# Performance work log

Measured on AMD Instinct MI355X. Metric: run time of the kernel, lower is better.

Reference implementation:

```python
import jax, jax.numpy as jnp
import numpy as np

N = 100000
E = 3200000
F_IN = 512
HID = 16
NUM_CLASSES = 2
NUM_GRAPHS = 256


def setup_inputs() -> dict:
    key = jax.random.key(0)
    k = jax.random.split(key, 8)
    x = jax.random.normal(k[0], (N, F_IN), dtype=jnp.float32)
    edge_index = jax.random.randint(k[1], (2, E), 0, N, dtype=jnp.int64)
    batch = jnp.sort(jax.random.randint(k[2], (N,), 0, NUM_GRAPHS, dtype=jnp.int64))
    # Glorot init like PyG GCNConv, biases zero-init
    W1 = jax.random.normal(k[3], (F_IN, HID), dtype=jnp.float32) * (2.0 / (F_IN + HID)) ** 0.5
    b1 = jnp.zeros((HID,), dtype=jnp.float32)
    W2 = jax.random.normal(k[4], (HID, NUM_CLASSES), dtype=jnp.float32) * (2.0 / (HID + NUM_CLASSES)) ** 0.5
    b2 = jnp.zeros((NUM_CLASSES,), dtype=jnp.float32)
    return {"x": x, "W1": W1, "b1": b1, "W2": W2, "b2": b2,
            "edge_index": edge_index, "batch": batch}


def _gcn_conv(x, W, b, src, dst, n):
    # PyG GCNConv: linear first, add self loops, symmetric deg^-1/2 normalization,
    # scatter-add messages from src to dst, then bias.
    h = x @ W                                        # [N, out]
    loops = jnp.arange(n, dtype=src.dtype)
    s = jnp.concatenate([src, loops])                # [E+N]
    d = jnp.concatenate([dst, loops])                # [E+N]
    deg = jax.ops.segment_sum(jnp.ones_like(d, dtype=h.dtype), d, num_segments=n)
    dinv = jax.lax.rsqrt(deg)                        # deg >= 1 due to self loops
    norm = dinv[s] * dinv[d]                         # [E+N]
    out = jax.ops.segment_sum(norm[:, None] * h[s], d, num_segments=n)
    return out + b


def reference(x, W1, b1, W2, b2, edge_index, batch):
    src, dst = edge_index[0], edge_index[1]
    h = jax.nn.relu(_gcn_conv(x, W1, b1, src, dst, N))
    h = _gcn_conv(h, W2, b2, src, dst, N)
    # global_mean_pool over graph ids
    sums = jax.ops.segment_sum(h, batch, num_segments=NUM_GRAPHS)
    counts = jax.ops.segment_sum(jnp.ones((N,), dtype=h.dtype), batch, num_segments=NUM_GRAPHS)
    pooled = sums / jnp.maximum(counts, 1.0)[:, None]  # [G, num_classes]
    return jax.nn.log_softmax(pooled, axis=1)
```

## Files before the change

### kernel.cpp

```cpp
#include <hip/hip_runtime.h>
#include <hip/hip_fp16.h>

#define N_NODES 100000
#define N_EDGES 3200000
#define F_INN 512
#define NGR 256
#define BSH 6
#define NBIN 1563
#define KBB 256
#define CHUNK (N_EDGES / KBB)
#define CAP 2560

typedef __attribute__((ext_vector_type(8))) short bf16x8;
typedef __attribute__((ext_vector_type(4))) float f32x4;

__device__ __forceinline__ uint f2bf2(float a, float b) {
  uint ua = __float_as_uint(a), ub = __float_as_uint(b);
  uint ra = (ua + 0x7FFF + ((ua >> 16) & 1)) >> 16;
  uint rb = (ub + 0x7FFF + ((ub >> 16) & 1)) >> 16;
  return ra | (rb << 16);
}

__global__ __launch_bounds__(512) void k_bin(const int* __restrict__ ei,
                                             int* __restrict__ bincur,
                                             int* __restrict__ rec,
                                             const float* __restrict__ W,
                                             ushort* __restrict__ Wt) {
  if (blockIdx.x == KBB) {
    for (int tid = threadIdx.x; tid < 16 * 512; tid += 512) {
      int n = tid >> 9;
      int k = tid & 511;
      uint u = __float_as_uint(W[k * 16 + n]);
      Wt[tid] = (ushort)((u + 0x7FFF + ((u >> 16) & 1)) >> 16);
    }
    return;
  }
  __shared__ int h[NBIN];
  __shared__ int base[NBIN];
  for (int t = threadIdx.x; t < NBIN; t += 512) h[t] = 0;
  __syncthreads();
  int e0 = blockIdx.x * CHUNK;
  for (int i = threadIdx.x; i < CHUNK; i += 512)
    atomicAdd(&h[ei[N_EDGES + e0 + i] >> BSH], 1);
  __syncthreads();
  for (int t = threadIdx.x; t < NBIN; t += 512) {
    int c = h[t];
    base[t] = t * CAP + (c ? atomicAdd(&bincur[t], c) : 0);
    h[t] = 0;
  }
  __syncthreads();
  for (int i = threadIdx.x; i < CHUNK; i += 512) {
    int s = ei[e0 + i];
    int d = ei[N_EDGES + e0 + i];
    int k = d >> BSH;
    int pos = base[k] + atomicAdd(&h[k], 1);
    rec[pos] = (s << BSH) | (d & 63);
  }
}

__global__ __launch_bounds__(256) void k_binsort(const int* __restrict__ rec,
                                                 const int* __restrict__ bincur,
                                                 int* __restrict__ rec2,
                                                 int* __restrict__ nstart,
                                                 int* __restrict__ ncnt,
                                                 float* __restrict__ dinv) {
  __shared__ int h[64], excl[64], cur[64];
  int k = blockIdx.x, t = threadIdx.x;
  if (t < 64) h[t] = 0;
  __syncthreads();
  int start = k * CAP;
  int end = start + bincur[k];
  for (int r = start + t; r < end; r += 256)
    atomicAdd(&h[rec[r] & 63], 1);
  __syncthreads();
  if (t < 64) {
    int v = h[t];
    int sc = v;
#pragma unroll
    for (int o = 1; o < 64; o <<= 1) {
      int u = __shfl_up(sc, o);
      if (t >= o) sc += u;
    }
    int ex = sc - v;
    excl[t] = ex;
    cur[t] = 0;
    int node = (k << BSH) + t;
    if (node < N_NODES) {
      nstart[node] = start + ex;
      ncnt[node] = v;
      dinv[node] = rsqrtf((float)v + 1.0f);
    }
  }
  __syncthreads();
  for (int r = start + t; r < end; r += 256) {
    int v = rec[r];
    int dl = v & 63;
    int pos = start + excl[dl] + atomicAdd(&cur[dl], 1);
    rec2[pos] = v;
  }
}

__global__ __launch_bounds__(256) void k_gemm1(const float* __restrict__ X,
                                               const ushort* __restrict__ Wt,
                                               const float* __restrict__ dinv,
                                               __half* __restrict__ T1h) {
  const int t = threadIdx.x;
  const int lane = t & 63;
  const int w = t >> 6;
  const int c16 = lane & 15;
  const int g = lane >> 4;
  const int arow = blockIdx.x * 64 + w * 16 + c16;
  const bool rv = arow < N_NODES;
  const float* xrow = X + (size_t)arow * F_INN + g * 8;
  const ushort* brow = Wt + c16 * 512 + g * 8;

  f32x4 acc = {0.f, 0.f, 0.f, 0.f};
#pragma unroll
  for (int ks = 0; ks < 16; ++ks) {
    float4 v0 = rv ? *(const float4*)(xrow + ks * 32)     : make_float4(0.f, 0.f, 0.f, 0.f);
    float4 v1 = rv ? *(const float4*)(xrow + ks * 32 + 4) : make_float4(0.f, 0.f, 0.f, 0.f);
    uint au[4] = { f2bf2(v0.x, v0.y), f2bf2(v0.z, v0.w),
                   f2bf2(v1.x, v1.y), f2bf2(v1.z, v1.w) };
    bf16x8 a = *(const bf16x8*)au;
    bf16x8 b = *(const bf16x8*)(brow + ks * 32);
    acc = __builtin_amdgcn_mfma_f32_16x16x32_bf16(a, b, acc, 0, 0, 0);
  }

  int rbase = blockIdx.x * 64 + w * 16 + g * 4;
#pragma unroll
  for (int j = 0; j < 4; ++j) {
    int r = rbase + j;
    if (r < N_NODES)
      T1h[(size_t)r * 16 + c16] = __float2half(dinv[r] * acc[j]);
  }
}

__global__ __launch_bounds__(256) void k_agg1(const int* __restrict__ rec2,
                                              const int* __restrict__ bincur,
                                              const int* __restrict__ nstart,
                                              const int* __restrict__ ncnt,
                                              const float* __restrict__ dinv,
                                              const __half* __restrict__ T1h,
                                              const float* __restrict__ b1,
                                              const float* __restrict__ W2,
                                              float* __restrict__ T2) {
  __shared__ float accs[64 * 17];
  __shared__ int recs[CAP];
  int k = blockIdx.x, t = threadIdx.x;
  int n0 = k << BSH;
  int cnt = bincur[k];
  for (int i = t; i < cnt; i += 256) recs[i] = rec2[k * CAP + i];
  int node = n0 + (t >> 2);
  int q = t & 3;
  bool nvalid = node < N_NODES;
  float a0 = 0.f, a1 = 0.f, a2 = 0.f, a3 = 0.f;
  int r = 0, e = 0;
  if (nvalid) {
    r = nstart[node] - k * CAP;
    e = r + ncnt[node];
    uint2 u = *(const uint2*)(T1h + (size_t)node * 16 + q * 4);
    float2 f0 = __half22float2(*reinterpret_cast<__half2*>(&u.x));
    float2 f1 = __half22float2(*reinterpret_cast<__half2*>(&u.y));
    a0 = f0.x; a1 = f0.y; a2 = f1.x; a3 = f1.y;
  }
  __syncthreads();
  for (; r + 1 < e; r += 2) {
    int v0 = recs[r], v1 = recs[r + 1];
    uint2 ua = *(const uint2*)(T1h + (size_t)(v0 >> BSH) * 16 + q * 4);
    uint2 ub = *(const uint2*)(T1h + (size_t)(v1 >> BSH) * 16 + q * 4);
    float2 fa0 = __half22float2(*reinterpret_cast<__half2*>(&ua.x));
    float2 fa1 = __half22float2(*reinterpret_cast<__half2*>(&ua.y));
    float2 fb0 = __half22float2(*reinterpret_cast<__half2*>(&ub.x));
    float2 fb1 = __half22float2(*reinterpret_cast<__half2*>(&ub.y));
    a0 += fa0.x + fb0.x; a1 += fa0.y + fb0.y;
    a2 += fa1.x + fb1.x; a3 += fa1.y + fb1.y;
  }
  if (r < e) {
    int v = recs[r];
    uint2 u = *(const uint2*)(T1h + (size_t)(v >> BSH) * 16 + q * 4);
    float2 f0 = __half22float2(*reinterpret_cast<__half2*>(&u.x));
    float2 f1 = __half22float2(*reinterpret_cast<__half2*>(&u.y));
    a0 += f0.x; a1 += f0.y; a2 += f1.x; a3 += f1.y;
  }
  float dd = nvalid ? dinv[node] : 0.f;
  float* rowp = &accs[(t >> 2) * 17 + q * 4];
  rowp[0] = dd * a0; rowp[1] = dd * a1; rowp[2] = dd * a2; rowp[3] = dd * a3;
  __syncthreads();
  if (t < 64) {
    int n = n0 + t;
    if (n < N_NODES) {
      float dd2 = dinv[n];
      float s0 = 0.f, s1 = 0.f;
#pragma unroll
      for (int c = 0; c < 16; ++c) {
        float hv = fmaxf(accs[t * 17 + c] + b1[c], 0.f);
        s0 = fmaf(hv, W2[c * 2 + 0], s0);
        s1 = fmaf(hv, W2[c * 2 + 1], s1);
      }
      T2[(size_t)n * 2 + 0] = dd2 * s0;
      T2[(size_t)n * 2 + 1] = dd2 * s1;
    }
  }
}

__global__ __launch_bounds__(128) void k_agg2(const int* __restrict__ rec2,
                                              const int* __restrict__ bincur,
                                              const int* __restrict__ nstart,
                                              const int* __restrict__ ncnt,
                                              const float* __restrict__ dinv,
                                              const float* __restrict__ T2,
                                              const int* __restrict__ batch,
                                              float* __restrict__ pool,
                                              float* __restrict__ gcnt) {
  __shared__ int recs[CAP];
  __shared__ float sm[128];
  int k = blockIdx.x, t = threadIdx.x;
  int n0 = k << BSH;
  int cnt = bincur[k];
  for (int i = t; i < cnt; i += 128) recs[i] = rec2[k * CAP + i];
  int node = n0 + (t >> 1);
  int c = t & 1;
  bool nvalid = node < N_NODES;
  float acc = 0.f;
  int r = 0, e = 0;
  if (nvalid) {
    r = nstart[node] - k * CAP;
    e = r + ncnt[node];
    acc = T2[(size_t)node * 2 + c];
  }
  __syncthreads();
  for (; r + 1 < e; r += 2) {
    int v0 = recs[r], v1 = recs[r + 1];
    acc += T2[(size_t)(v0 >> BSH) * 2 + c] + T2[(size_t)(v1 >> BSH) * 2 + c];
  }
  if (r < e) acc += T2[(size_t)(recs[r] >> BSH) * 2 + c];
  sm[t] = nvalid ? dinv[node] * acc : 0.f;
  __syncthreads();
  if (t < 64) {
    int n = n0 + t;
    bool valid = n < N_NODES;
    int b = valid ? batch[n] : -1;
    float vx = sm[2 * t], vy = sm[2 * t + 1];
    int b0 = __shfl(b, 0);
    if (__all(b == b0)) {
      if (b0 >= 0) {
#pragma unroll
        for (int o = 32; o > 0; o >>= 1) {
          vx += __shfl_xor(vx, o);
          vy += __shfl_xor(vy, o);
        }
        if (t == 0) {
          atomicAdd(&pool[b0 * 2 + 0], vx);
          atomicAdd(&pool[b0 * 2 + 1], vy);
          atomicAdd(&gcnt[b0], 64.0f);
        }
      }
    } else if (valid) {
      atomicAdd(&pool[b * 2 + 0], vx);
      atomicAdd(&pool[b * 2 + 1], vy);
      atomicAdd(&gcnt[b], 1.0f);
    }
  }
}

__global__ __launch_bounds__(256) void k_final(const float* __restrict__ pool,
                                               const float* __restrict__ gcnt,
                                               const float* __restrict__ b2,
                                               float* __restrict__ out) {
  int g = threadIdx.x;
  if (g < NGR) {
    float c = fmaxf(gcnt[g], 1.0f);
    float p0 = pool[g * 2 + 0] / c + b2[0];
    float p1 = pool[g * 2 + 1] / c + b2[1];
    float m = fmaxf(p0, p1);
    float l = logf(expf(p0 - m) + expf(p1 - m));
    out[g * 2 + 0] = p0 - m - l;
    out[g * 2 + 1] = p1 - m - l;
  }
}

extern "C" void kernel_launch(void* const* d_in, const int* in_sizes, int n_in,
                              void* d_out, int out_size, void* d_ws, size_t ws_size,
                              hipStream_t stream) {
  const float* x  = (const float*)d_in[0];
  const float* W1 = (const float*)d_in[1];
  const float* b1 = (const float*)d_in[2];
  const float* W2 = (const float*)d_in[3];
  const float* b2 = (const float*)d_in[4];
  const int*   ei = (const int*)d_in[5];
  const int*   bt = (const int*)d_in[6];
  float* out = (float*)d_out;

  char* ws = (char*)d_ws;
  int*   bincur = (int*)ws;    ws += (size_t)NBIN * 4;
  float* pool   = (float*)ws;  ws += 2 * NGR * 4;
  float* gcnt   = (float*)ws;  ws += NGR * 4;
  int*   nstart = (int*)ws;    ws += (size_t)N_NODES * 4;
  int*   ncnt   = (int*)ws;    ws += (size_t)N_NODES * 4;
  float* dinv   = (float*)ws;  ws += (size_t)N_NODES * 4;
  ushort* wt    = (ushort*)ws; ws += (size_t)16 * 512 * 2;
  int*   rec    = (int*)ws;    ws += (size_t)NBIN * CAP * 4;
  int*   rec2   = (int*)ws;    ws += (size_t)NBIN * CAP * 4;
  __half* t1h   = (__half*)ws; ws += (size_t)N_NODES * 16 * 2;
  float* t2     = (float*)ws;  ws += (size_t)N_NODES * 2 * 4;

  hipMemsetAsync(bincur, 0, (size_t)(NBIN + 3 * NGR) * 4, stream);

  k_bin    <<<KBB + 1, 512, 0, stream>>>(ei, bincur, rec, W1, wt);
  k_binsort<<<NBIN, 256, 0, stream>>>(rec, bincur, rec2, nstart, ncnt, dinv);
  k_gemm1  <<<NBIN, 256, 0, stream>>>(x, wt, dinv, t1h);
  k_agg1   <<<NBIN, 256, 0, stream>>>(rec2, bincur, nstart, ncnt, dinv, t1h, b1, W2, t2);
  k_agg2   <<<NBIN, 128, 0, stream>>>(rec2, bincur, nstart, ncnt, dinv, t2, bt, pool, gcnt);
  k_final  <<<1, 256, 0, stream>>>(pool, gcnt, b2, out);
}
```

Baseline: 201.7 us.

## Drop per-node bin sort; aggregate edges with LDS atomics per bin

Removes the k_binsort pass, which built a per-node CSR order (rec2, nstart, dinv). Degree counts now come from global atomics in k_bin, and dinv is recomputed from ncnt wherever it is needed. Both aggregation kernels walk the unsorted bin records edge-parallel and accumulate into shared-memory node rows with LDS float atomics. This saves a kernel launch plus a full read and write of the edge records, at the cost of 3.2M global atomics in k_bin and LDS atomic contention during aggregation.

After: 565.3 us. 2.8x slower.

```diff
diff --git a/kernel.cpp b/kernel.cpp
--- a/kernel.cpp
+++ b/kernel.cpp
@@ -24,6 +24,7 @@
 __global__ __launch_bounds__(512) void k_bin(const int* __restrict__ ei,
                                              int* __restrict__ bincur,
                                              int* __restrict__ rec,
+                                             int* __restrict__ ncnt,
                                              const float* __restrict__ W,
                                              ushort* __restrict__ Wt) {
   if (blockIdx.x == KBB) {
@@ -55,54 +56,13 @@
     int k = d >> BSH;
     int pos = base[k] + atomicAdd(&h[k], 1);
     rec[pos] = (s << BSH) | (d & 63);
-  }
-}
-
-__global__ __launch_bounds__(256) void k_binsort(const int* __restrict__ rec,
-                                                 const int* __restrict__ bincur,
-                                                 int* __restrict__ rec2,
-                                                 int* __restrict__ nstart,
-                                                 int* __restrict__ ncnt,
-                                                 float* __restrict__ dinv) {
-  __shared__ int h[64], excl[64], cur[64];
-  int k = blockIdx.x, t = threadIdx.x;
-  if (t < 64) h[t] = 0;
-  __syncthreads();
-  int start = k * CAP;
-  int end = start + bincur[k];
-  for (int r = start + t; r < end; r += 256)
-    atomicAdd(&h[rec[r] & 63], 1);
-  __syncthreads();
-  if (t < 64) {
-    int v = h[t];
-    int sc = v;
-#pragma unroll
-    for (int o = 1; o < 64; o <<= 1) {
-      int u = __shfl_up(sc, o);
-      if (t >= o) sc += u;
-    }
-    int ex = sc - v;
-    excl[t] = ex;
-    cur[t] = 0;
-    int node = (k << BSH) + t;
-    if (node < N_NODES) {
-      nstart[node] = start + ex;
-      ncnt[node] = v;
-      dinv[node] = rsqrtf((float)v + 1.0f);
-    }
-  }
-  __syncthreads();
-  for (int r = start + t; r < end; r += 256) {
-    int v = rec[r];
-    int dl = v & 63;
-    int pos = start + excl[dl] + atomicAdd(&cur[dl], 1);
-    rec2[pos] = v;
+    atomicAdd(&ncnt[d], 1);
   }
 }
 
 __global__ __launch_bounds__(256) void k_gemm1(const float* __restrict__ X,
                                                const ushort* __restrict__ Wt,
-                                               const float* __restrict__ dinv,
+                                               const int* __restrict__ ncnt,
                                                __half* __restrict__ T1h) {
   const int t = threadIdx.x;
   const int lane = t & 63;
@@ -130,16 +90,16 @@
 #pragma unroll
   for (int j = 0; j < 4; ++j) {
     int r = rbase + j;
-    if (r < N_NODES)
-      T1h[(size_t)r * 16 + c16] = __float2half(dinv[r] * acc[j]);
-  }
-}
-
-__global__ __launch_bounds__(256) void k_agg1(const int* __restrict__ rec2,
+    if (r < N_NODES) {
+      float di = rsqrtf((float)ncnt[r] + 1.0f);
+      T1h[(size_t)r * 16 + c16] = __float2half(di * acc[j]);
+    }
+  }
+}
+
+__global__ __launch_bounds__(256) void k_agg1(const int* __restrict__ rec,
                                               const int* __restrict__ bincur,
-                                              const int* __restrict__ nstart,
                                               const int* __restrict__ ncnt,
-                                              const float* __restrict__ dinv,
                                               const __half* __restrict__ T1h,
                                               const float* __restrict__ b1,
                                               const float* __restrict__ W2,
@@ -149,98 +109,102 @@
   int k = blockIdx.x, t = threadIdx.x;
   int n0 = k << BSH;
   int cnt = bincur[k];
-  for (int i = t; i < cnt; i += 256) recs[i] = rec2[k * CAP + i];
+  for (int i = t; i < cnt; i += 256) recs[i] = rec[k * CAP + i];
   int node = n0 + (t >> 2);
   int q = t & 3;
-  bool nvalid = node < N_NODES;
-  float a0 = 0.f, a1 = 0.f, a2 = 0.f, a3 = 0.f;
-  int r = 0, e = 0;
-  if (nvalid) {
-    r = nstart[node] - k * CAP;
-    e = r + ncnt[node];
-    uint2 u = *(const uint2*)(T1h + (size_t)node * 16 + q * 4);
-    float2 f0 = __half22float2(*reinterpret_cast<__half2*>(&u.x));
-    float2 f1 = __half22float2(*reinterpret_cast<__half2*>(&u.y));
-    a0 = f0.x; a1 = f0.y; a2 = f1.x; a3 = f1.y;
-  }
-  __syncthreads();
-  for (; r + 1 < e; r += 2) {
-    int v0 = recs[r], v1 = recs[r + 1];
+  {
+    float* rowp = &accs[(t >> 2) * 17 + q * 4];
+    if (node < N_NODES) {
+      uint2 u = *(const uint2*)(T1h + (size_t)node * 16 + q * 4);
+      float2 f0 = __half22float2(*reinterpret_cast<__half2*>(&u.x));
+      float2 f1 = __half22float2(*reinterpret_cast<__half2*>(&u.y));
+      rowp[0] = f0.x; rowp[1] = f0.y; rowp[2] = f1.x; rowp[3] = f1.y;
+    } else {
+      rowp[0] = rowp[1] = rowp[2] = rowp[3] = 0.f;
+    }
+  }
+  __syncthreads();
+  int i = t >> 2;
+  for (; i + 64 < cnt; i += 128) {
+    int v0 = recs[i], v1 = recs[i + 64];
     uint2 ua = *(const uint2*)(T1h + (size_t)(v0 >> BSH) * 16 + q * 4);
     uint2 ub = *(const uint2*)(T1h + (size_t)(v1 >> BSH) * 16 + q * 4);
     float2 fa0 = __half22float2(*reinterpret_cast<__half2*>(&ua.x));
     float2 fa1 = __half22float2(*reinterpret_cast<__half2*>(&ua.y));
     float2 fb0 = __half22float2(*reinterpret_cast<__half2*>(&ub.x));
     float2 fb1 = __half22float2(*reinterpret_cast<__half2*>(&ub.y));
-    a0 += fa0.x + fb0.x; a1 += fa0.y + fb0.y;
-    a2 += fa1.x + fb1.x; a3 += fa1.y + fb1.y;
-  }
-  if (r < e) {
-    int v = recs[r];
+    float* a0p = &accs[(v0 & 63) * 17 + q * 4];
+    float* a1p = &accs[(v1 & 63) * 17 + q * 4];
+    atomicAdd(a0p + 0, fa0.x); atomicAdd(a0p + 1, fa0.y);
+    atomicAdd(a0p + 2, fa1.x); atomicAdd(a0p + 3, fa1.y);
+    atomicAdd(a1p + 0, fb0.x); atomicAdd(a1p + 1, fb0.y);
+    atomicAdd(a1p + 2, fb1.x); atomicAdd(a1p + 3, fb1.y);
+  }
+  if (i < cnt) {
+    int v = recs[i];
     uint2 u = *(const uint2*)(T1h + (size_t)(v >> BSH) * 16 + q * 4);
     float2 f0 = __half22float2(*reinterpret_cast<__half2*>(&u.x));
     float2 f1 = __half22float2(*reinterpret_cast<__half2*>(&u.y));
-    a0 += f0.x; a1 += f0.y; a2 += f1.x; a3 += f1.y;
-  }
-  float dd = nvalid ? dinv[node] : 0.f;
-  float* rowp = &accs[(t >> 2) * 17 + q * 4];
-  rowp[0] = dd * a0; rowp[1] = dd * a1; rowp[2] = dd * a2; rowp[3] = dd * a3;
+    float* ap = &accs[(v & 63) * 17 + q * 4];
+    atomicAdd(ap + 0, f0.x); atomicAdd(ap + 1, f0.y);
+    atomicAdd(ap + 2, f1.x); atomicAdd(ap + 3, f1.y);
+  }
   __syncthreads();
   if (t < 64) {
     int n = n0 + t;
     if (n < N_NODES) {
-      float dd2 = dinv[n];
+      float dd = rsqrtf((float)ncnt[n] + 1.0f);
       float s0 = 0.f, s1 = 0.f;
 #pragma unroll
       for (int c = 0; c < 16; ++c) {
-        float hv = fmaxf(accs[t * 17 + c] + b1[c], 0.f);
+        float hv = fmaxf(fmaf(dd, accs[t * 17 + c], b1[c]), 0.f);
         s0 = fmaf(hv, W2[c * 2 + 0], s0);
         s1 = fmaf(hv, W2[c * 2 + 1], s1);
       }
-      T2[(size_t)n * 2 + 0] = dd2 * s0;
-      T2[(size_t)n * 2 + 1] = dd2 * s1;
-    }
-  }
-}
-
-__global__ __launch_bounds__(128) void k_agg2(const int* __restrict__ rec2,
+      T2[(size_t)n * 2 + 0] = dd * s0;
+      T2[(size_t)n * 2 + 1] = dd * s1;
+    }
+  }
+}
+
+__global__ __launch_bounds__(256) void k_agg2(const int* __restrict__ rec,
                                               const int* __restrict__ bincur,
-                                              const int* __restrict__ nstart,
                                               const int* __restrict__ ncnt,
-                                              const float* __restrict__ dinv,
                                               const float* __restrict__ T2,
                                               const int* __restrict__ batch,
                                               float* __restrict__ pool,
                                               float* __restrict__ gcnt) {
   __shared__ int recs[CAP];
-  __shared__ float sm[128];
+  __shared__ float sm[64 * 3];
   int k = blockIdx.x, t = threadIdx.x;
   int n0 = k << BSH;
   int cnt = bincur[k];
-  for (int i = t; i < cnt; i += 128) recs[i] = rec2[k * CAP + i];
-  int node = n0 + (t >> 1);
+  for (int i = t; i < cnt; i += 256) recs[i] = rec[k * CAP + i];
+  if (t < 128) {
+    int n = n0 + (t >> 1), c = t & 1;
+    sm[(t >> 1) * 3 + c] = (n < N_NODES) ? T2[(size_t)n * 2 + c] : 0.f;
+  }
+  __syncthreads();
   int c = t & 1;
-  bool nvalid = node < N_NODES;
-  float acc = 0.f;
-  int r = 0, e = 0;
-  if (nvalid) {
-    r = nstart[node] - k * CAP;
-    e = r + ncnt[node];
-    acc = T2[(size_t)node * 2 + c];
-  }
-  __syncthreads();
-  for (; r + 1 < e; r += 2) {
-    int v0 = recs[r], v1 = recs[r + 1];
-    acc += T2[(size_t)(v0 >> BSH) * 2 + c] + T2[(size_t)(v1 >> BSH) * 2 + c];
-  }
-  if (r < e) acc += T2[(size_t)(recs[r] >> BSH) * 2 + c];
-  sm[t] = nvalid ? dinv[node] * acc : 0.f;
+  int i = t >> 1;
+  for (; i + 128 < cnt; i += 256) {
+    int v0 = recs[i], v1 = recs[i + 128];
+    float u0 = T2[(size_t)(v0 >> BSH) * 2 + c];
+    float u1 = T2[(size_t)(v1 >> BSH) * 2 + c];
+    atomicAdd(&sm[(v0 & 63) * 3 + c], u0);
+    atomicAdd(&sm[(v1 & 63) * 3 + c], u1);
+  }
+  if (i < cnt) {
+    int v = recs[i];
+    atomicAdd(&sm[(v & 63) * 3 + c], T2[(size_t)(v >> BSH) * 2 + c]);
+  }
   __syncthreads();
   if (t < 64) {
     int n = n0 + t;
     bool valid = n < N_NODES;
+    float dd = valid ? rsqrtf((float)ncnt[n] + 1.0f) : 0.f;
     int b = valid ? batch[n] : -1;
-    float vx = sm[2 * t], vy = sm[2 * t + 1];
+    float vx = dd * sm[t * 3 + 0], vy = dd * sm[t * 3 + 1];
     int b0 = __shfl(b, 0);
     if (__all(b == b0)) {
       if (b0 >= 0) {
@@ -295,21 +259,17 @@
   int*   bincur = (int*)ws;    ws += (size_t)NBIN * 4;
   float* pool   = (float*)ws;  ws += 2 * NGR * 4;
   float* gcnt   = (float*)ws;  ws += NGR * 4;
-  int*   nstart = (int*)ws;    ws += (size_t)N_NODES * 4;
   int*   ncnt   = (int*)ws;    ws += (size_t)N_NODES * 4;
-  float* dinv   = (float*)ws;  ws += (size_t)N_NODES * 4;
   ushort* wt    = (ushort*)ws; ws += (size_t)16 * 512 * 2;
   int*   rec    = (int*)ws;    ws += (size_t)NBIN * CAP * 4;
-  int*   rec2   = (int*)ws;    ws += (size_t)NBIN * CAP * 4;
   __half* t1h   = (__half*)ws; ws += (size_t)N_NODES * 16 * 2;
   float* t2     = (float*)ws;  ws += (size_t)N_NODES * 2 * 4;
 
-  hipMemsetAsync(bincur, 0, (size_t)(NBIN + 3 * NGR) * 4, stream);
-
-  k_bin    <<<KBB + 1, 512, 0, stream>>>(ei, bincur, rec, W1, wt);
-  k_binsort<<<NBIN, 256, 0, stream>>>(rec, bincur, rec2, nstart, ncnt, dinv);
-  k_gemm1  <<<NBIN, 256, 0, stream>>>(x, wt, dinv, t1h);
-  k_agg1   <<<NBIN, 256, 0, stream>>>(rec2, bincur, nstart, ncnt, dinv, t1h, b1, W2, t2);
-  k_agg2   <<<NBIN, 128, 0, stream>>>(rec2, bincur, nstart, ncnt, dinv, t2, bt, pool, gcnt);
-  k_final  <<<1, 256, 0, stream>>>(pool, gcnt, b2, out);
-}
+  hipMemsetAsync(bincur, 0, (size_t)(NBIN + 3 * NGR + N_NODES) * 4, stream);
+
+  k_bin   <<<KBB + 1, 512, 0, stream>>>(ei, bincur, rec, ncnt, W1, wt);
+  k_gemm1 <<<NBIN, 256, 0, stream>>>(x, wt, ncnt, t1h);
+  k_agg1  <<<NBIN, 256, 0, stream>>>(rec, bincur, ncnt, t1h, b1, W2, t2);
+  k_agg2  <<<NBIN, 256, 0, stream>>>(rec, bincur, ncnt, t2, bt, pool, gcnt);
+  k_final <<<1, 256, 0, stream>>>(pool, gcnt, b2, out);
+}
```
